# Optimization experiments

Measured on AMD Instinct MI355X. Metric: run time of the kernel, lower is better.

## Reference

```python
import jax, jax.numpy as jnp
import numpy as np
from jax.scipy.special import logsumexp

TEMPERATURE = 0.05
HARD_NEG_WEIGHT = 1.0
MARGIN = 0.2
EXPLICIT_NEG_WEIGHT = 2.0
NEG_INF = -1e9


def setup_inputs() -> dict:
    key = jax.random.key(0)
    k1, k2, k3 = jax.random.split(key, 3)
    N, D = 8192, 512
    return {
        "asm_embeddings": jax.random.normal(k1, (N, D), dtype=jnp.float32),
        "source_embeddings": jax.random.normal(k2, (N, D), dtype=jnp.float32),
        "labels": jax.random.randint(k3, (N,), 0, 2, dtype=jnp.int64),
    }


def reference(asm_embeddings, source_embeddings, labels):
    # L2-normalize both embedding sets
    a = asm_embeddings / jnp.linalg.norm(asm_embeddings, axis=1, keepdims=True)
    s = source_embeddings / jnp.linalg.norm(source_embeddings, axis=1, keepdims=True)
    sim = jnp.matmul(a, s.T) / TEMPERATURE  # [N, N]

    N = labels.shape[0]
    pos_mask = labels == 1
    neg_mask = labels == 0
    num_pos = jnp.sum(pos_mask).astype(sim.dtype)
    num_neg = jnp.sum(neg_mask)

    # column weights: explicit negatives (label==0) get EXPLICIT_NEG_WEIGHT,
    # others 1; the positive (diagonal) logit always has weight 1.
    log_w = jnp.log(jnp.where(neg_mask, EXPLICIT_NEG_WEIGHT, 1.0).astype(sim.dtype))
    eye = jnp.eye(N, dtype=bool)
    weighted_logits = sim + jnp.where(eye, 0.0, log_w[None, :])  # [N, N]

    lse = logsumexp(weighted_logits, axis=1)  # weighted logsumexp per row
    diag = jnp.diagonal(sim)
    per_row_loss = lse - diag  # -log_prob_pos

    infonce = jnp.sum(jnp.where(pos_mask, per_row_loss, 0.0)) / num_pos

    # margin penalty on hardest explicit-negative diagonal similarity
    mean_pos_sim = jnp.sum(jnp.where(pos_mask, diag, 0.0)) / num_pos
    hard_neg_sim = jnp.max(jnp.where(neg_mask, diag, NEG_INF))
    penalty = jax.nn.relu(hard_neg_sim - mean_pos_sim + MARGIN)
    penalty = jnp.where(num_neg > 0, penalty, 0.0)

    return infonce + HARD_NEG_WEIGHT * penalty
```

## Files before the change

kernel.cpp:

```cpp
#include <hip/hip_runtime.h>
#include <math.h>

#define NROWS 8192
#define DIM 512
#define INV_T 20.0f
#define QS 500.0f
#define DEQ2 (INV_T * 1.4426950408889634f / (QS * QS))

typedef __attribute__((ext_vector_type(4))) int i32x4;

__device__ __forceinline__ void gload_lds16(const void* g, void* l) {
    __builtin_amdgcn_global_load_lds(
        (const __attribute__((address_space(1))) unsigned int*)g,
        (__attribute__((address_space(3))) unsigned int*)l, 16, 0, 0);
}

__device__ __forceinline__ void block_bar() {
    asm volatile("" ::: "memory");
    __builtin_amdgcn_s_barrier();
    asm volatile("" ::: "memory");
}

__device__ __forceinline__ float hw_exp2(float x) {
    float r;
    asm("v_exp_f32 %0, %1" : "=v"(r) : "v"(x));
    return r;
}

__device__ __forceinline__ float dot4(float4 a, float4 b) {
    return a.x * b.x + a.y * b.y + a.z * b.z + a.w * b.w;
}

__device__ __forceinline__ int q4(float4 v, float s) {
    int b0 = __float2int_rn(fminf(fmaxf(v.x * s, -127.f), 127.f)) & 255;
    int b1 = __float2int_rn(fminf(fmaxf(v.y * s, -127.f), 127.f)) & 255;
    int b2 = __float2int_rn(fminf(fmaxf(v.z * s, -127.f), 127.f)) & 255;
    int b3 = __float2int_rn(fminf(fmaxf(v.w * s, -127.f), 127.f)) & 255;
    return b0 | (b1 << 8) | (b2 << 16) | (b3 << 24);
}

__global__ __launch_bounds__(256) void norm_kernel(
    const float* __restrict__ A, const float* __restrict__ S,
    const int* __restrict__ labels, signed char* __restrict__ aQ,
    signed char* __restrict__ sQ, float* __restrict__ diag,
    float* __restrict__ lw2) {
    const int wave = threadIdx.x >> 6, lane = threadIdx.x & 63;
    const int row = blockIdx.x * 4 + wave;
    const float4* a4 = (const float4*)(A + (size_t)row * DIM);
    const float4* s4 = (const float4*)(S + (size_t)row * DIM);
    float4 a0 = a4[lane], a1 = a4[lane + 64];
    float4 s0 = s4[lane], s1 = s4[lane + 64];
    float saa = dot4(a0, a0) + dot4(a1, a1);
    float sss = dot4(s0, s0) + dot4(s1, s1);
    float sas = dot4(a0, s0) + dot4(a1, s1);
    for (int m = 1; m < 64; m <<= 1) {
        saa += __shfl_xor(saa, m);
        sss += __shfl_xor(sss, m);
        sas += __shfl_xor(sas, m);
    }
    const float ra = rsqrtf(saa), rs = rsqrtf(sss);
    signed char* arow = aQ + (size_t)row * DIM;
    signed char* srow = sQ + (size_t)row * DIM;
    *(int*)(arow + lane * 4)       = q4(a0, ra * QS);
    *(int*)(arow + 256 + lane * 4) = q4(a1, ra * QS);
    *(int*)(srow + lane * 4)       = q4(s0, rs * QS);
    *(int*)(srow + 256 + lane * 4) = q4(s1, rs * QS);
    if (lane == 0) {
        diag[row] = sas * ra * rs * INV_T;
        lw2[row] = (labels[row] == 0) ? 1.0f : 0.0f;
    }
}

__global__ __launch_bounds__(1024) void compact_kernel(
    const int* __restrict__ labels, int* __restrict__ perm,
    float* __restrict__ lsum, int* __restrict__ meta) {
    const int tid = threadIdx.x;
    for (int i = tid; i < 8448; i += 1024) {
        perm[i] = 0;
        lsum[i] = 0.f;
    }
    __syncthreads();
    const int lane = tid & 63, wid = tid >> 6;
    int lab[8], cnt = 0;
#pragma unroll
    for (int i = 0; i < 8; ++i) {
        lab[i] = labels[tid * 8 + i];
        cnt += (lab[i] == 1);
    }
    int inc = cnt;
    for (int d = 1; d < 64; d <<= 1) {
        int v = __shfl_up(inc, d);
        if (lane >= d) inc += v;
    }
    __shared__ int wsum[16], wpre[16];
    if (lane == 63) wsum[wid] = inc;
    __syncthreads();
    if (tid == 0) {
        int acc = 0;
        for (int w = 0; w < 16; ++w) { acc += wsum[w]; wpre[w] = acc; }
    }
    __syncthreads();
    int off = (wid ? wpre[wid - 1] : 0) + inc - cnt;
#pragma unroll
    for (int i = 0; i < 8; ++i)
        if (lab[i] == 1) perm[off++] = tid * 8 + i;
    if (tid == 0) {
        meta[0] = wpre[15];
        meta[1] = (wpre[15] + 255) >> 8;
    }
}

__global__ __launch_bounds__(512, 4) void lse_gemm(
    const signed char* __restrict__ Aq, const signed char* __restrict__ Bq,
    const float* __restrict__ lw2, const int* __restrict__ perm,
    const int* __restrict__ meta, float* __restrict__ lsum) {
    __shared__ __align__(16) char lds[49152];

    const int bid = blockIdx.x;
    const int rt = bid >> 4, ctg = bid & 15;
    if (rt >= meta[1]) return;
    const int row0 = rt * 256;
    const int colg = ctg * 512;

    const int tid = threadIdx.x;
    const int wid = tid >> 6, lane = tid & 63;
    const int wr = wid >> 1, wc = wid & 1;
    const int fr = lane & 15, grp = lane >> 4;

    const int sl = (tid & 3) ^ ((tid >> 3) & 3);
    const int r0 = perm[row0 + (tid >> 2)];
    const int r1 = perm[row0 + 128 + (tid >> 2)];
    const signed char* aSrc0 = Aq + (size_t)r0 * DIM + sl * 16;
    const signed char* aSrc1 = Aq + (size_t)r1 * DIM + sl * 16;
    const signed char* bSrc = Bq + (size_t)(colg + (tid >> 2)) * DIM + sl * 16;
    char* dstA = lds + tid * 16;
    char* dstB = lds + 16384 + tid * 16;

#define STAGE(buf, TT)                                                        \
    do {                                                                      \
        const int ct_ = (TT) >> 3, k_ = (TT) & 7;                             \
        gload_lds16(aSrc0 + k_ * 64,              dstA + (buf) * 24576);      \
        gload_lds16(aSrc1 + k_ * 64,              dstA + (buf) * 24576 + 8192); \
        gload_lds16(bSrc + ct_ * 65536 + k_ * 64, dstB + (buf) * 24576);      \
    } while (0)

    const int ps = (grp ^ ((fr >> 1) & 3)) << 4;
    const char* rdA = lds + (wr * 64 + fr) * 64 + ps;
    const char* rdB = lds + 16384 + (wc * 64 + fr) * 64 + ps;

    STAGE(0, 0);

    i32x4 acc[4][4] = {};
#pragma unroll 2
    for (int T = 0; T < 32; ++T) {
        const int buf = T & 1;
        if (T < 31) {
            STAGE(buf ^ 1, T + 1);
            asm volatile("s_waitcnt vmcnt(3)" ::: "memory");
        } else {
            asm volatile("s_waitcnt vmcnt(0)" ::: "memory");
        }
        block_bar();

        i32x4 a[4], b[4];
#pragma unroll
        for (int m = 0; m < 4; ++m)
            a[m] = *(const i32x4*)(rdA + buf * 24576 + m * 1024);
#pragma unroll
        for (int n = 0; n < 4; ++n)
            b[n] = *(const i32x4*)(rdB + buf * 24576 + n * 1024);
        asm volatile("s_waitcnt lgkmcnt(0)" ::: "memory");
        __builtin_amdgcn_sched_barrier(0);

        __builtin_amdgcn_s_setprio(1);
#pragma unroll
        for (int m = 0; m < 4; ++m)
#pragma unroll
            for (int n = 0; n < 4; ++n)
                acc[m][n] = __builtin_amdgcn_mfma_i32_16x16x64_i8(
                    a[m], b[n], acc[m][n], 0, 0, 0);
        __builtin_amdgcn_s_setprio(0);

        if ((T & 7) == 7) {
            const int ct = T >> 3;
            const int col0 = colg + ct * 128 + wc * 64;
            float lwv[4];
#pragma unroll
            for (int n = 0; n < 4; ++n)
                lwv[n] = lw2[col0 + n * 16 + fr];
#pragma unroll
            for (int m = 0; m < 4; ++m)
#pragma unroll
                for (int j = 0; j < 4; ++j) {
                    float s = 0.f;
#pragma unroll
                    for (int n = 0; n < 4; ++n)
                        s += hw_exp2(fmaf((float)acc[m][n][j], DEQ2, lwv[n]));
                    s += __shfl_xor(s, 1);
                    s += __shfl_xor(s, 2);
                    s += __shfl_xor(s, 4);
                    s += __shfl_xor(s, 8);
                    if (fr == 0)
                        atomicAdd(&lsum[row0 + wr * 64 + m * 16 + grp * 4 + j], s);
                }
#pragma unroll
            for (int m = 0; m < 4; ++m)
#pragma unroll
                for (int n = 0; n < 4; ++n)
                    acc[m][n] = i32x4{0, 0, 0, 0};
        }
        block_bar();
    }
#undef STAGE
}

__global__ __launch_bounds__(1024) void finalize_kernel(
    const float* __restrict__ lsum, const float* __restrict__ diag,
    const int* __restrict__ labels, const int* __restrict__ perm,
    const int* __restrict__ meta, float* __restrict__ out) {
    const int tid = threadIdx.x;
    const int npos = meta[0];
    float sl = 0.f, sd = 0.f, mx = -1e9f;
    int nn_ = 0;
    for (int c = tid; c < npos; c += 1024) {
        const int r = perm[c];
        const float dg = diag[r];
        sl += logf(lsum[c]) - dg;
        sd += dg;
    }
    for (int i = tid; i < NROWS; i += 1024) {
        if (labels[i] == 0) {
            nn_++;
            mx = fmaxf(mx, diag[i]);
        }
    }
    for (int m = 1; m < 64; m <<= 1) {
        sl += __shfl_xor(sl, m);
        sd += __shfl_xor(sd, m);
        mx = fmaxf(mx, __shfl_xor(mx, m));
        nn_ += __shfl_xor(nn_, m);
    }
    __shared__ float rsl[16], rsd[16], rmx[16];
    __shared__ int rnn[16];
    const int wave = tid >> 6, lane = tid & 63;
    if (lane == 0) {
        rsl[wave] = sl; rsd[wave] = sd; rmx[wave] = mx; rnn[wave] = nn_;
    }
    __syncthreads();
    if (tid == 0) {
        float SL = 0.f, SD = 0.f, MX = -1e9f;
        int NN = 0;
        for (int w = 0; w < 16; w++) {
            SL += rsl[w]; SD += rsd[w]; MX = fmaxf(MX, rmx[w]); NN += rnn[w];
        }
        const float infonce = SL / (float)npos;
        const float meanpos = SD / (float)npos;
        float pen = fmaxf(MX - meanpos + 0.2f, 0.0f);
        if (NN == 0) pen = 0.0f;
        out[0] = infonce + pen;
    }
}

extern "C" void kernel_launch(void* const* d_in, const int* in_sizes, int n_in,
                              void* d_out, int out_size, void* d_ws, size_t ws_size,
                              hipStream_t stream) {
    const float* A = (const float*)d_in[0];
    const float* S = (const float*)d_in[1];
    const int* labels = (const int*)d_in[2];
    float* out = (float*)d_out;

    char* ws = (char*)d_ws;
    signed char* aQ = (signed char*)ws;
    signed char* sQ = (signed char*)(ws + (size_t)NROWS * DIM);
    char* p = ws + (size_t)NROWS * DIM * 2;
    float* diag = (float*)p;
    float* lw2 = (float*)(p + 32768);
    float* lsum = (float*)(p + 65536);
    int* perm = (int*)(p + 65536 + 36864);
    int* meta = (int*)(p + 65536 + 73728);

    norm_kernel<<<NROWS / 4, 256, 0, stream>>>(A, S, labels, aQ, sQ, diag, lw2);
    compact_kernel<<<1, 1024, 0, stream>>>(labels, perm, lsum, meta);
    lse_gemm<<<512, 512, 0, stream>>>(aQ, sQ, lw2, perm, meta, lsum);
    finalize_kernel<<<1, 1024, 0, stream>>>(lsum, diag, labels, perm, meta, out);
}
```

Baseline: 56.31 us.

## Enlarge GEMM tile to 256x256 with K=128 stages and split A/B prefetch

The int8 LSE GEMM now has each block compute a 256-row by 256-column tile per step with K chunks of 128. LDS grows to 128KB, double-buffered, with an XOR swizzle over 8 slots. Each wave holds 8x4 accumulators, and the A and B prefetches for the next chunk are issued between sub-steps of the MFMA work. The goal is higher arithmetic intensity and fewer LDS loads and barriers per MFMA. In exchange, occupancy drops to 2 blocks, register pressure rises, and each iteration carries more barriers.

```diff
diff --git a/kernel.cpp b/kernel.cpp
--- a/kernel.cpp
+++ b/kernel.cpp
@@ -110,11 +110,11 @@
     }
 }
 
-__global__ __launch_bounds__(512, 4) void lse_gemm(
+__global__ __launch_bounds__(512, 2) void lse_gemm(
     const signed char* __restrict__ Aq, const signed char* __restrict__ Bq,
     const float* __restrict__ lw2, const int* __restrict__ perm,
     const int* __restrict__ meta, float* __restrict__ lsum) {
-    __shared__ __align__(16) char lds[49152];
+    __shared__ __align__(16) char lds[131072];
 
     const int bid = blockIdx.x;
     const int rt = bid >> 4, ctg = bid & 15;
@@ -124,54 +124,65 @@
 
     const int tid = threadIdx.x;
     const int wid = tid >> 6, lane = tid & 63;
-    const int wr = wid >> 1, wc = wid & 1;
+    const int wr = wid >> 2, wc = wid & 3;
     const int fr = lane & 15, grp = lane >> 4;
-
-    const int sl = (tid & 3) ^ ((tid >> 3) & 3);
-    const int r0 = perm[row0 + (tid >> 2)];
-    const int r1 = perm[row0 + 128 + (tid >> 2)];
-    const signed char* aSrc0 = Aq + (size_t)r0 * DIM + sl * 16;
-    const signed char* aSrc1 = Aq + (size_t)r1 * DIM + sl * 16;
-    const signed char* bSrc = Bq + (size_t)(colg + (tid >> 2)) * DIM + sl * 16;
-    char* dstA = lds + tid * 16;
-    char* dstB = lds + 16384 + tid * 16;
-
-#define STAGE(buf, TT)                                                        \
+    const int f7 = fr & 7;
+
+    const int sl = (tid & 7) ^ ((tid >> 3) & 7);
+    const signed char* aSrcs[4];
+#pragma unroll
+    for (int ra = 0; ra < 4; ++ra)
+        aSrcs[ra] = Aq +
+            (size_t)perm[row0 + ra * 64 + (tid >> 3)] * DIM + sl * 16;
+    const signed char* bSrc =
+        Bq + (size_t)(colg + (tid >> 3)) * DIM + sl * 16;
+    char* dst = lds + tid * 16;
+
+#define STAGE_A4(buf, TT)                                                     \
     do {                                                                      \
-        const int ct_ = (TT) >> 3, k_ = (TT) & 7;                             \
-        gload_lds16(aSrc0 + k_ * 64,              dstA + (buf) * 24576);      \
-        gload_lds16(aSrc1 + k_ * 64,              dstA + (buf) * 24576 + 8192); \
-        gload_lds16(bSrc + ct_ * 65536 + k_ * 64, dstB + (buf) * 24576);      \
+        _Pragma("unroll")                                                     \
+        for (int ra = 0; ra < 4; ++ra)                                        \
+            gload_lds16(aSrcs[ra] + ((TT) & 3) * 128,                         \
+                        dst + (buf) * 65536 + ra * 8192);                     \
     } while (0)
-
-    const int ps = (grp ^ ((fr >> 1) & 3)) << 4;
-    const char* rdA = lds + (wr * 64 + fr) * 64 + ps;
-    const char* rdB = lds + 16384 + (wc * 64 + fr) * 64 + ps;
-
-    STAGE(0, 0);
-
-    i32x4 acc[4][4] = {};
-#pragma unroll 2
-    for (int T = 0; T < 32; ++T) {
-        const int buf = T & 1;
-        if (T < 31) {
-            STAGE(buf ^ 1, T + 1);
-            asm volatile("s_waitcnt vmcnt(3)" ::: "memory");
-        } else {
-            asm volatile("s_waitcnt vmcnt(0)" ::: "memory");
-        }
-        block_bar();
-
-        i32x4 a[4], b[4];
-#pragma unroll
-        for (int m = 0; m < 4; ++m)
-            a[m] = *(const i32x4*)(rdA + buf * 24576 + m * 1024);
+#define STAGE_B4(buf, TT)                                                     \
+    do {                                                                      \
+        _Pragma("unroll")                                                     \
+        for (int rb = 0; rb < 4; ++rb)                                        \
+            gload_lds16(bSrc + ((TT) >> 2) * 131072 + rb * 32768 +            \
+                            ((TT) & 3) * 128,                                 \
+                        dst + (buf) * 65536 + 32768 + rb * 8192);             \
+    } while (0)
+
+    const char* rdA = lds + (wr * 128 + fr) * 128;
+    const char* rdB = lds + 32768 + (wc * 64 + fr) * 128;
+    const int psk0 = ((0 * 4 + grp) ^ f7) << 4;
+    const int psk1 = ((1 * 4 + grp) ^ f7) << 4;
+
+    STAGE_A4(0, 0);
+    STAGE_B4(0, 0);
+    asm volatile("s_waitcnt vmcnt(0)" ::: "memory");
+    block_bar();
+
+    i32x4 a[4], b[4];
+    i32x4 acc[8][4] = {};
+
+#pragma unroll 1
+    for (int tt = 0; tt < 8; ++tt) {
+        const int buf = tt & 1, nbuf = buf ^ 1;
+        const char* bA = rdA + buf * 65536;
+        const char* bB = rdB + buf * 65536;
+
+#pragma unroll
+        for (int m = 0; m < 4; ++m)
+            a[m] = *(const i32x4*)(bA + m * 2048 + psk0);
 #pragma unroll
         for (int n = 0; n < 4; ++n)
-            b[n] = *(const i32x4*)(rdB + buf * 24576 + n * 1024);
+            b[n] = *(const i32x4*)(bB + n * 2048 + psk0);
+        if (tt < 7) STAGE_A4(nbuf, tt + 1);
+        block_bar();
         asm volatile("s_waitcnt lgkmcnt(0)" ::: "memory");
         __builtin_amdgcn_sched_barrier(0);
-
         __builtin_amdgcn_s_setprio(1);
 #pragma unroll
         for (int m = 0; m < 4; ++m)
@@ -180,16 +191,70 @@
                 acc[m][n] = __builtin_amdgcn_mfma_i32_16x16x64_i8(
                     a[m], b[n], acc[m][n], 0, 0, 0);
         __builtin_amdgcn_s_setprio(0);
-
-        if ((T & 7) == 7) {
-            const int ct = T >> 3;
-            const int col0 = colg + ct * 128 + wc * 64;
+        block_bar();
+
+#pragma unroll
+        for (int m = 0; m < 4; ++m)
+            a[m] = *(const i32x4*)(bA + (m + 4) * 2048 + psk0);
+        if (tt < 7) STAGE_B4(nbuf, tt + 1);
+        block_bar();
+        asm volatile("s_waitcnt lgkmcnt(0)" ::: "memory");
+        __builtin_amdgcn_sched_barrier(0);
+        __builtin_amdgcn_s_setprio(1);
+#pragma unroll
+        for (int m = 0; m < 4; ++m)
+#pragma unroll
+            for (int n = 0; n < 4; ++n)
+                acc[m + 4][n] = __builtin_amdgcn_mfma_i32_16x16x64_i8(
+                    a[m], b[n], acc[m + 4][n], 0, 0, 0);
+        __builtin_amdgcn_s_setprio(0);
+        block_bar();
+
+#pragma unroll
+        for (int m = 0; m < 4; ++m)
+            a[m] = *(const i32x4*)(bA + m * 2048 + psk1);
+#pragma unroll
+        for (int n = 0; n < 4; ++n)
+            b[n] = *(const i32x4*)(bB + n * 2048 + psk1);
+        block_bar();
+        asm volatile("s_waitcnt lgkmcnt(0)" ::: "memory");
+        __builtin_amdgcn_sched_barrier(0);
+        __builtin_amdgcn_s_setprio(1);
+#pragma unroll
+        for (int m = 0; m < 4; ++m)
+#pragma unroll
+            for (int n = 0; n < 4; ++n)
+                acc[m][n] = __builtin_amdgcn_mfma_i32_16x16x64_i8(
+                    a[m], b[n], acc[m][n], 0, 0, 0);
+        __builtin_amdgcn_s_setprio(0);
+        block_bar();
+
+#pragma unroll
+        for (int m = 0; m < 4; ++m)
+            a[m] = *(const i32x4*)(bA + (m + 4) * 2048 + psk1);
+        asm volatile("s_waitcnt vmcnt(0)" ::: "memory");
+        block_bar();
+        asm volatile("s_waitcnt lgkmcnt(0)" ::: "memory");
+        __builtin_amdgcn_sched_barrier(0);
+        __builtin_amdgcn_s_setprio(1);
+#pragma unroll
+        for (int m = 0; m < 4; ++m)
+#pragma unroll
+            for (int n = 0; n < 4; ++n)
+                acc[m + 4][n] = __builtin_amdgcn_mfma_i32_16x16x64_i8(
+                    a[m], b[n], acc[m + 4][n], 0, 0, 0);
+        __builtin_amdgcn_s_setprio(0);
+        block_bar();
+
+        if ((tt & 3) == 3) {
+            const int ct = tt >> 2;
+            const int col0 = colg + ct * 256 + wc * 64;
             float lwv[4];
 #pragma unroll
             for (int n = 0; n < 4; ++n)
                 lwv[n] = lw2[col0 + n * 16 + fr];
 #pragma unroll
-            for (int m = 0; m < 4; ++m)
+            for (int m = 0; m < 8; ++m)
 #pragma unroll
                 for (int j = 0; j < 4; ++j) {
                     float s = 0.f;
@@ -201,17 +266,17 @@
                     s += __shfl_xor(s, 4);
                     s += __shfl_xor(s, 8);
                     if (fr == 0)
-                        atomicAdd(&lsum[row0 + wr * 64 + m * 16 + grp * 4 + j], s);
+                        atomicAdd(&lsum[row0 + wr * 128 + m * 16 + grp * 4 + j], s);
                 }
 #pragma unroll
-            for (int m = 0; m < 4; ++m)
+            for (int m = 0; m < 8; ++m)
 #pragma unroll
                 for (int n = 0; n < 4; ++n)
                     acc[m][n] = i32x4{0, 0, 0, 0};
         }
-        block_bar();
-    }
-#undef STAGE
+    }
+#undef STAGE_A4
+#undef STAGE_B4
 }
 
 __global__ __launch_bounds__(1024) void finalize_kernel(
```

Result: slower. 59.05 us (+4.9%).
